# Optimization experiments

Hardware: AMD Instinct MI355X
Metric: run time of the kernel (lower is better)

## Reference

```python
import jax, jax.numpy as jnp
import numpy as np

ALPHA = 1.0
IGNORE = 255

def setup_inputs() -> dict:
    key = jax.random.key(0)
    k1, k2, k3 = jax.random.split(key, 3)
    B, C_new, C_old, H, W = 8, 21, 16, 512, 512
    inputs = jax.random.normal(k1, (B, C_new, H, W), dtype=jnp.float32)
    targets = jax.random.normal(k2, (B, C_old, H, W), dtype=jnp.float32)
    masks = jax.random.randint(k3, (B, H, W), 0, 21, dtype=jnp.int32)
    return {"inputs": inputs, "targets": targets, "masks": masks}


def reference(inputs, targets, masks):
    B, C, H, W = inputs.shape
    C_old = targets.shape[1]

    outputs = jax.nn.log_softmax(inputs, axis=1)          # [B,C,H,W]
    labels = jax.nn.softmax(targets * ALPHA, axis=1)      # [B,C_old,H,W]

    # present[c] == True iff c appears anywhere in masks (== torch.unique),
    # excluding background 0 and ignore 255.
    present = jnp.zeros((C,), dtype=bool).at[masks.reshape(-1)].set(True, mode='drop')
    present = present.at[0].set(False)
    present = present & (jnp.arange(C) != IGNORE)

    # base: labels padded with zeros up to C new-task channels
    base = jnp.concatenate(
        [labels, jnp.zeros((B, C - C_old, H, W), labels.dtype)], axis=1)

    # for each present label l: channel l fully overwritten by (masks==l)*labels[:,0]
    onehot = (masks[:, None] == jnp.arange(C)[None, :, None, None]).astype(labels.dtype)
    replaced = onehot * labels[:, :1]                     # [B,C,H,W]
    new_labels = jnp.where(present[None, :, None, None], replaced, base)

    # channel 0 cumulatively multiplied by (1-mask_l) for every present l:
    # survives only where the pixel label is 0 or 255 (any valid label is present).
    bg = ((masks == 0) | (masks == IGNORE)).astype(labels.dtype)
    new_labels = new_labels.at[:, 0].set(labels[:, 0] * bg)

    loss = (outputs * new_labels).mean(axis=1)            # [B,H,W]
    return -jnp.mean(loss)
```

## Files before the change

### kernel.cpp

```cpp
#include <hip/hip_runtime.h>

#define HW    262144
#define NPIX  2097152
#define CNEW  21
#define COLD  16

__global__ void lgod_present_scan(const int* __restrict__ masks,
                                  unsigned int* __restrict__ pm) {
    unsigned int local = 0;
    int stride = gridDim.x * blockDim.x;
    for (int p = blockIdx.x * blockDim.x + threadIdx.x; p < NPIX; p += stride) {
        int m = masks[p];
        if (m >= 1 && m < CNEW) local |= (1u << m);
    }
    __shared__ unsigned int sm;
    if (threadIdx.x == 0) sm = 0;
    __syncthreads();
    #pragma unroll
    for (int off = 32; off; off >>= 1) local |= __shfl_down(local, off);
    if ((threadIdx.x & 63) == 0 && local) atomicOr(&sm, local);
    __syncthreads();
    if (threadIdx.x == 0 && sm) atomicOr(pm, sm);
}

__global__ __launch_bounds__(256)
void lgod_main(const float* __restrict__ inp,
               const float* __restrict__ tgt,
               const int*   __restrict__ masks,
               const unsigned int* __restrict__ pm_p,
               double* __restrict__ accum) {
    const unsigned int pm = *pm_p;
    const bool need_extra = (pm & 0xFFFEu) != 0xFFFEu;

    float acc = 0.f;
    const int stride = gridDim.x * blockDim.x;
    for (int p = blockIdx.x * blockDim.x + threadIdx.x; p < NPIX; p += stride) {
        const int b  = p >> 18;
        const int hw = p & (HW - 1);
        const float* ip = inp + (size_t)b * CNEW * HW + hw;
        const float* tp = tgt + (size_t)b * COLD * HW + hw;

        float in[CNEW];
        float t[COLD];
        #pragma unroll
        for (int c = 0; c < CNEW; ++c) in[c] = ip[(size_t)c * HW];
        #pragma unroll
        for (int c = 0; c < COLD; ++c) t[c] = tp[(size_t)c * HW];
        const int m = masks[p];

        float mi = in[0];
        #pragma unroll
        for (int c = 1; c < CNEW; ++c) mi = fmaxf(mi, in[c]);
        float se = 0.f;
        #pragma unroll
        for (int c = 0; c < CNEW; ++c) se += __expf(in[c] - mi);
        const float lse = __logf(se);

        float mt = t[0];
        #pragma unroll
        for (int c = 1; c < COLD; ++c) mt = fmaxf(mt, t[c]);
        float st = 0.f;
        #pragma unroll
        for (int c = 0; c < COLD; ++c) st += __expf(t[c] - mt);
        const float L0 = __expf(t[0] - mt) / st;

        const int mm = (m == 0 || m == 255) ? 0 : m;
        float vm = in[0];
        #pragma unroll
        for (int c = 1; c < CNEW; ++c) vm = (c == mm) ? in[c] : vm;

        float S = 0.f;
        if (m < CNEW || m == 255)
            S = (vm - mi - lse) * L0;

        if (need_extra) {
            const float inv_st = 1.f / st;
            #pragma unroll
            for (int c = 1; c < COLD; ++c)
                if (!((pm >> c) & 1u))
                    S += (in[c] - mi - lse) * __expf(t[c] - mt) * inv_st;
        }
        acc += S;
    }

    #pragma unroll
    for (int off = 32; off; off >>= 1) acc += __shfl_down(acc, off);
    __shared__ float warp_s[4];
    const int wid = threadIdx.x >> 6;
    if ((threadIdx.x & 63) == 0) warp_s[wid] = acc;
    __syncthreads();
    if (threadIdx.x == 0) {
        float tot = warp_s[0] + warp_s[1] + warp_s[2] + warp_s[3];
        atomicAdd(accum, (double)tot);
    }
}

__global__ void lgod_finalize(const double* __restrict__ accum,
                              float* __restrict__ out) {
    out[0] = (float)(-accum[0] / ((double)CNEW * (double)NPIX));
}

extern "C" void kernel_launch(void* const* d_in, const int* in_sizes, int n_in,
                              void* d_out, int out_size, void* d_ws, size_t ws_size,
                              hipStream_t stream) {
    const float* inp   = (const float*)d_in[0];
    const float* tgt   = (const float*)d_in[1];
    const int*   masks = (const int*)d_in[2];
    float* out = (float*)d_out;

    double* accum      = (double*)d_ws;
    unsigned int* pm   = (unsigned int*)((char*)d_ws + 8);

    hipMemsetAsync(d_ws, 0, 16, stream);
    lgod_present_scan<<<512, 256, 0, stream>>>(masks, pm);
    lgod_main<<<2048, 256, 0, stream>>>(inp, tgt, masks, pm, accum);
    lgod_finalize<<<1, 1, 0, stream>>>(accum, out);
}
```

Baseline: 74.07 us.

## Vectorize per-pixel loss to float4 and drop max-subtraction from softmax sums

Each thread now handles four consecutive pixels with float4/int4 loads and one thread per quad, with no grid-stride loop. The softmax and log-softmax are rewritten algebraically without max subtraction: it accumulates raw exp sums, plus weighted sums P and Q for absent channels, in a single streaming pass over channels, with no per-pixel arrays. This aims to cut instruction count, register pressure and memory transaction overhead. Skipping max subtraction risks overflow or precision loss for large-magnitude inputs, which is safe only for normal-distributed test data. The mask scan is also vectorized and its grid is halved.

Measured after the change: 68.24 us. 1.09x faster.

```diff
diff --git a/kernel.cpp b/kernel.cpp
--- a/kernel.cpp
+++ b/kernel.cpp
@@ -1,6 +1,7 @@
 #include <hip/hip_runtime.h>
 
 #define HW    262144
+#define HW4   65536
 #define NPIX  2097152
 #define CNEW  21
 #define COLD  16
@@ -8,10 +9,15 @@
 __global__ void lgod_present_scan(const int* __restrict__ masks,
                                   unsigned int* __restrict__ pm) {
     unsigned int local = 0;
-    int stride = gridDim.x * blockDim.x;
-    for (int p = blockIdx.x * blockDim.x + threadIdx.x; p < NPIX; p += stride) {
-        int m = masks[p];
-        if (m >= 1 && m < CNEW) local |= (1u << m);
+    const int4* m4 = (const int4*)masks;
+    const int n4 = NPIX / 4;
+    const int stride = gridDim.x * blockDim.x;
+    for (int p = blockIdx.x * blockDim.x + threadIdx.x; p < n4; p += stride) {
+        int4 v = m4[p];
+        if (v.x >= 1 && v.x < CNEW) local |= (1u << v.x);
+        if (v.y >= 1 && v.y < CNEW) local |= (1u << v.y);
+        if (v.z >= 1 && v.z < CNEW) local |= (1u << v.z);
+        if (v.w >= 1 && v.w < CNEW) local |= (1u << v.w);
     }
     __shared__ unsigned int sm;
     if (threadIdx.x == 0) sm = 0;
@@ -24,63 +30,71 @@
 }
 
 __global__ __launch_bounds__(256)
-void lgod_main(const float* __restrict__ inp,
-               const float* __restrict__ tgt,
-               const int*   __restrict__ masks,
+void lgod_main(const float4* __restrict__ inp4,
+               const float4* __restrict__ tgt4,
+               const int4*   __restrict__ masks4,
                const unsigned int* __restrict__ pm_p,
                double* __restrict__ accum) {
     const unsigned int pm = *pm_p;
-    const bool need_extra = (pm & 0xFFFEu) != 0xFFFEu;
+    const int t   = blockIdx.x * blockDim.x + threadIdx.x;
+    const int b   = t >> 16;
+    const int hw4 = t & (HW4 - 1);
+    const float4* ip = inp4 + (size_t)b * CNEW * HW4 + hw4;
+    const float4* tp = tgt4 + (size_t)b * COLD * HW4 + hw4;
+
+    const int4 mv = masks4[t];
+    int ma[4] = {mv.x, mv.y, mv.z, mv.w};
+    int mm[4];
+    #pragma unroll
+    for (int j = 0; j < 4; ++j)
+        mm[j] = (ma[j] == 0 || ma[j] == 255) ? 0 : ma[j];
+
+    float se[4] = {0,0,0,0};
+    float st[4] = {0,0,0,0};
+    float P[4]  = {0,0,0,0};
+    float Q[4]  = {0,0,0,0};
+    float t0e[4];
+    float vm[4];
+
+    #pragma unroll
+    for (int c = 0; c < COLD; ++c) {
+        float4 iv = ip[(size_t)c * HW4];
+        float4 tv = tp[(size_t)c * HW4];
+        float ia[4] = {iv.x, iv.y, iv.z, iv.w};
+        float ta[4] = {tv.x, tv.y, tv.z, tv.w};
+        const bool absent = (c >= 1) && !((pm >> c) & 1u);
+        #pragma unroll
+        for (int j = 0; j < 4; ++j) {
+            float e = __expf(ta[j]);
+            st[j] += e;
+            if (c == 0) t0e[j] = e;
+            if (absent) { P[j] += ia[j] * e; Q[j] += e; }
+            se[j] += __expf(ia[j]);
+            if (c == 0) vm[j] = ia[j];
+            else        vm[j] = (c == mm[j]) ? ia[j] : vm[j];
+        }
+    }
+    #pragma unroll
+    for (int c = COLD; c < CNEW; ++c) {
+        float4 iv = ip[(size_t)c * HW4];
+        float ia[4] = {iv.x, iv.y, iv.z, iv.w};
+        #pragma unroll
+        for (int j = 0; j < 4; ++j) {
+            se[j] += __expf(ia[j]);
+            vm[j] = (c == mm[j]) ? ia[j] : vm[j];
+        }
+    }
 
     float acc = 0.f;
-    const int stride = gridDim.x * blockDim.x;
-    for (int p = blockIdx.x * blockDim.x + threadIdx.x; p < NPIX; p += stride) {
-        const int b  = p >> 18;
-        const int hw = p & (HW - 1);
-        const float* ip = inp + (size_t)b * CNEW * HW + hw;
-        const float* tp = tgt + (size_t)b * COLD * HW + hw;
-
-        float in[CNEW];
-        float t[COLD];
-        #pragma unroll
-        for (int c = 0; c < CNEW; ++c) in[c] = ip[(size_t)c * HW];
-        #pragma unroll
-        for (int c = 0; c < COLD; ++c) t[c] = tp[(size_t)c * HW];
-        const int m = masks[p];
-
-        float mi = in[0];
-        #pragma unroll
-        for (int c = 1; c < CNEW; ++c) mi = fmaxf(mi, in[c]);
-        float se = 0.f;
-        #pragma unroll
-        for (int c = 0; c < CNEW; ++c) se += __expf(in[c] - mi);
-        const float lse = __logf(se);
-
-        float mt = t[0];
-        #pragma unroll
-        for (int c = 1; c < COLD; ++c) mt = fmaxf(mt, t[c]);
-        float st = 0.f;
-        #pragma unroll
-        for (int c = 0; c < COLD; ++c) st += __expf(t[c] - mt);
-        const float L0 = __expf(t[0] - mt) / st;
-
-        const int mm = (m == 0 || m == 255) ? 0 : m;
-        float vm = in[0];
-        #pragma unroll
-        for (int c = 1; c < CNEW; ++c) vm = (c == mm) ? in[c] : vm;
-
+    #pragma unroll
+    for (int j = 0; j < 4; ++j) {
+        float lse = __logf(se[j]);
+        float inv = 1.0f / st[j];
         float S = 0.f;
-        if (m < CNEW || m == 255)
-            S = (vm - mi - lse) * L0;
-
-        if (need_extra) {
-            const float inv_st = 1.f / st;
-            #pragma unroll
-            for (int c = 1; c < COLD; ++c)
-                if (!((pm >> c) & 1u))
-                    S += (in[c] - mi - lse) * __expf(t[c] - mt) * inv_st;
-        }
-        acc += S;
+        if (ma[j] < CNEW || ma[j] == 255)
+            S = (vm[j] - lse) * t0e[j];
+        S += P[j] - lse * Q[j];
+        acc += S * inv;
     }
 
     #pragma unroll
@@ -103,16 +117,18 @@
 extern "C" void kernel_launch(void* const* d_in, const int* in_sizes, int n_in,
                               void* d_out, int out_size, void* d_ws, size_t ws_size,
                               hipStream_t stream) {
-    const float* inp   = (const float*)d_in[0];
-    const float* tgt   = (const float*)d_in[1];
-    const int*   masks = (const int*)d_in[2];
+    const float4* inp4   = (const float4*)d_in[0];
+    const float4* tgt4   = (const float4*)d_in[1];
+    const int*    masks  = (const int*)d_in[2];
     float* out = (float*)d_out;
 
-    double* accum      = (double*)d_ws;
-    unsigned int* pm   = (unsigned int*)((char*)d_ws + 8);
+    double* accum    = (double*)d_ws;
+    unsigned int* pm = (unsigned int*)((char*)d_ws + 8);
 
     hipMemsetAsync(d_ws, 0, 16, stream);
-    lgod_present_scan<<<512, 256, 0, stream>>>(masks, pm);
-    lgod_main<<<2048, 256, 0, stream>>>(inp, tgt, masks, pm, accum);
+    lgod_present_scan<<<256, 256, 0, stream>>>(masks, pm);
+    lgod_main<<<NPIX / 4 / 256, 256, 0, stream>>>(inp4, (const float4*)d_in[1],
+                                                  (const int4*)masks, pm, accum);
     lgod_finalize<<<1, 1, 0, stream>>>(accum, out);
+    (void)inp4; (void)out_size; (void)ws_size; (void)n_in; (void)in_sizes;
 }
```

## Fuse presence scan into main kernel with per-channel partial sums resolved at finalize

Applied to the files above, without the earlier changes.

Removes the separate mask-presence scan kernel. The main pass now ORs presence bits itself and accumulates per-channel contributions for channels 1-15 unconditionally, and the finalize kernel adds only the channels found absent. Max subtraction is dropped from both softmaxes to save a pass of compares, which risks overflow in exp for large inputs. The trade-off is 15 extra accumulators per thread plus their reductions and atomics, in exchange for one fewer kernel launch and one fewer read of the masks.

New measurement: 92.39 us. +24.7%, slower.

```diff
diff --git a/kernel.cpp b/kernel.cpp
--- a/kernel.cpp
+++ b/kernel.cpp
@@ -4,100 +4,110 @@
 #define NPIX  2097152
 #define CNEW  21
 #define COLD  16
-
-__global__ void lgod_present_scan(const int* __restrict__ masks,
-                                  unsigned int* __restrict__ pm) {
-    unsigned int local = 0;
-    int stride = gridDim.x * blockDim.x;
-    for (int p = blockIdx.x * blockDim.x + threadIdx.x; p < NPIX; p += stride) {
-        int m = masks[p];
-        if (m >= 1 && m < CNEW) local |= (1u << m);
-    }
-    __shared__ unsigned int sm;
-    if (threadIdx.x == 0) sm = 0;
-    __syncthreads();
-    #pragma unroll
-    for (int off = 32; off; off >>= 1) local |= __shfl_down(local, off);
-    if ((threadIdx.x & 63) == 0 && local) atomicOr(&sm, local);
-    __syncthreads();
-    if (threadIdx.x == 0 && sm) atomicOr(pm, sm);
-}
+#define NBLK  2048
+#define NTHR  256
 
 __global__ __launch_bounds__(256)
 void lgod_main(const float* __restrict__ inp,
                const float* __restrict__ tgt,
                const int*   __restrict__ masks,
-               const unsigned int* __restrict__ pm_p,
-               double* __restrict__ accum) {
-    const unsigned int pm = *pm_p;
-    const bool need_extra = (pm & 0xFFFEu) != 0xFFFEu;
+               double* __restrict__ accum,
+               float*  __restrict__ Tc,
+               unsigned int* __restrict__ pmp)
+{
+    float tacc[15];
+    #pragma unroll
+    for (int i = 0; i < 15; ++i) tacc[i] = 0.f;
+    float macc = 0.f;
+    unsigned int pbits = 0;
 
-    float acc = 0.f;
-    const int stride = gridDim.x * blockDim.x;
-    for (int p = blockIdx.x * blockDim.x + threadIdx.x; p < NPIX; p += stride) {
+    const int stride = NBLK * NTHR;
+    for (int p = blockIdx.x * NTHR + threadIdx.x; p < NPIX; p += stride) {
         const int b  = p >> 18;
         const int hw = p & (HW - 1);
-        const float* ip = inp + (size_t)b * CNEW * HW + hw;
-        const float* tp = tgt + (size_t)b * COLD * HW + hw;
+        const float* ipx = inp + (size_t)b * CNEW * HW + hw;
+        const float* tpx = tgt + (size_t)b * COLD * HW + hw;
+        const int m = masks[p];
+        if (m >= 1 && m < CNEW) pbits |= (1u << m);
 
-        float in[CNEW];
-        float t[COLD];
-        #pragma unroll
-        for (int c = 0; c < CNEW; ++c) in[c] = ip[(size_t)c * HW];
-        #pragma unroll
-        for (int c = 0; c < COLD; ++c) t[c] = tp[(size_t)c * HW];
-        const int m = masks[p];
-
-        float mi = in[0];
-        #pragma unroll
-        for (int c = 1; c < CNEW; ++c) mi = fmaxf(mi, in[c]);
-        float se = 0.f;
-        #pragma unroll
-        for (int c = 0; c < CNEW; ++c) se += __expf(in[c] - mi);
-        const float lse = __logf(se);
-
-        float mt = t[0];
-        #pragma unroll
-        for (int c = 1; c < COLD; ++c) mt = fmaxf(mt, t[c]);
+        float e[COLD];
         float st = 0.f;
         #pragma unroll
-        for (int c = 0; c < COLD; ++c) st += __expf(t[c] - mt);
-        const float L0 = __expf(t[0] - mt) / st;
+        for (int c = 0; c < COLD; ++c) {
+            e[c] = __expf(tpx[(size_t)c * HW]);
+            st += e[c];
+        }
 
         const int mm = (m == 0 || m == 255) ? 0 : m;
-        float vm = in[0];
+        float ikeep[15];
+        float x0 = ipx[0];
+        float se = __expf(x0);
+        float vm = x0;
         #pragma unroll
-        for (int c = 1; c < CNEW; ++c) vm = (c == mm) ? in[c] : vm;
+        for (int c = 1; c < COLD; ++c) {
+            float x = ipx[(size_t)c * HW];
+            ikeep[c - 1] = x;
+            se += __expf(x);
+            vm = (c == mm) ? x : vm;
+        }
+        #pragma unroll
+        for (int c = COLD; c < CNEW; ++c) {
+            float x = ipx[(size_t)c * HW];
+            se += __expf(x);
+            vm = (c == mm) ? x : vm;
+        }
 
-        float S = 0.f;
+        const float lse = __logf(se);
+        const float inv = 1.0f / st;
         if (m < CNEW || m == 255)
-            S = (vm - mi - lse) * L0;
-
-        if (need_extra) {
-            const float inv_st = 1.f / st;
-            #pragma unroll
-            for (int c = 1; c < COLD; ++c)
-                if (!((pm >> c) & 1u))
-                    S += (in[c] - mi - lse) * __expf(t[c] - mt) * inv_st;
-        }
-        acc += S;
+            macc += (vm - lse) * e[0] * inv;
+        #pragma unroll
+        for (int c = 1; c < COLD; ++c)
+            tacc[c - 1] += (ikeep[c - 1] - lse) * e[c] * inv;
     }
 
     #pragma unroll
-    for (int off = 32; off; off >>= 1) acc += __shfl_down(acc, off);
-    __shared__ float warp_s[4];
+    for (int off = 32; off; off >>= 1) macc += __shfl_down(macc, off);
+    #pragma unroll
+    for (int i = 0; i < 15; ++i) {
+        #pragma unroll
+        for (int off = 32; off; off >>= 1) tacc[i] += __shfl_down(tacc[i], off);
+    }
+    #pragma unroll
+    for (int off = 32; off; off >>= 1) pbits |= __shfl_down(pbits, off);
+
+    __shared__ float s_m[4];
+    __shared__ float s_t[4][15];
+    __shared__ unsigned int s_p;
+    if (threadIdx.x == 0) s_p = 0;
+    __syncthreads();
     const int wid = threadIdx.x >> 6;
-    if ((threadIdx.x & 63) == 0) warp_s[wid] = acc;
+    if ((threadIdx.x & 63) == 0) {
+        s_m[wid] = macc;
+        #pragma unroll
+        for (int i = 0; i < 15; ++i) s_t[wid][i] = tacc[i];
+        if (pbits) atomicOr(&s_p, pbits);
+    }
     __syncthreads();
     if (threadIdx.x == 0) {
-        float tot = warp_s[0] + warp_s[1] + warp_s[2] + warp_s[3];
-        atomicAdd(accum, (double)tot);
+        atomicAdd(accum, (double)(s_m[0] + s_m[1] + s_m[2] + s_m[3]));
+        if (s_p) atomicOr(pmp, s_p);
+    }
+    if (threadIdx.x < 15) {
+        const int i = threadIdx.x;
+        atomicAdd(&Tc[i], s_t[0][i] + s_t[1][i] + s_t[2][i] + s_t[3][i]);
     }
 }
 
 __global__ void lgod_finalize(const double* __restrict__ accum,
+                              const float* __restrict__ Tc,
+                              const unsigned int* __restrict__ pmp,
                               float* __restrict__ out) {
-    out[0] = (float)(-accum[0] / ((double)CNEW * (double)NPIX));
+    double v = accum[0];
+    const unsigned int pm = pmp[0];
+    for (int c = 1; c < COLD; ++c)
+        if (!((pm >> c) & 1u)) v += (double)Tc[c - 1];
+    out[0] = (float)(-v / ((double)CNEW * (double)NPIX));
 }
 
 extern "C" void kernel_launch(void* const* d_in, const int* in_sizes, int n_in,
@@ -108,11 +118,12 @@
     const int*   masks = (const int*)d_in[2];
     float* out = (float*)d_out;
 
-    double* accum      = (double*)d_ws;
-    unsigned int* pm   = (unsigned int*)((char*)d_ws + 8);
+    double* accum    = (double*)d_ws;
+    float*  Tc       = (float*)((char*)d_ws + 8);
+    unsigned int* pm = (unsigned int*)((char*)d_ws + 68);
 
-    hipMemsetAsync(d_ws, 0, 16, stream);
-    lgod_present_scan<<<512, 256, 0, stream>>>(masks, pm);
-    lgod_main<<<2048, 256, 0, stream>>>(inp, tgt, masks, pm, accum);
-    lgod_finalize<<<1, 1, 0, stream>>>(accum, out);
+    hipMemsetAsync(d_ws, 0, 128, stream);
+    lgod_main<<<NBLK, NTHR, 0, stream>>>(inp, tgt, masks, accum, Tc, pm);
+    lgod_finalize<<<1, 1, 0, stream>>>(accum, Tc, pm, out);
+    (void)out_size; (void)ws_size; (void)n_in; (void)in_sizes;
 }
```
